# Optimization experiments

Hardware: AMD Instinct MI355X
Metric: run time of the kernel (lower is better)

## Reference

```python
import jax, jax.numpy as jnp
import numpy as np

B, T = 128, 512          # batch, sequence length (padded game length)
F_IN = 19 * 19           # flattened Go board features
H = 128                  # n_hid
P = 19 * 19 + 1          # policy classes: board points + pass


def setup_inputs() -> dict:
    key = jax.random.key(0)
    ks = jax.random.split(key, 8)
    s = 0.05  # init scale
    return {
        "states": jax.random.normal(ks[0], (B, T, F_IN), jnp.float32),
        "moves": jax.random.randint(ks[1], (B, T), 0, P, jnp.int32),
        "values": jax.random.uniform(ks[2], (B, T), jnp.float32, -1.0, 1.0),
        # LSTM layer 0: concat([x, h]) @ W0 + b0, gates [i, f, g, o]
        "W0": jax.random.normal(ks[3], (F_IN + H, 4 * H), jnp.float32) * s,
        "b0": jnp.zeros((4 * H,), jnp.float32),
        # LSTM layer 1
        "W1": jax.random.normal(ks[4], (H + H, 4 * H), jnp.float32) * s,
        "b1": jnp.zeros((4 * H,), jnp.float32),
        # policy head (size**2 + 1 logits), value head (tanh scalar)
        "Wp": jax.random.normal(ks[5], (H, P), jnp.float32) * s,
        "bp": jnp.zeros((P,), jnp.float32),
        "Wv": jax.random.normal(ks[6], (H, 1), jnp.float32) * s,
        "bv": jnp.zeros((1,), jnp.float32),
    }


def _lstm_cell(h, c, x, W, b):
    # TF LSTMCell: z = [x; h] @ W + b, forget bias 1.0
    z = jnp.concatenate([x, h], axis=-1) @ W + b
    i, f, g, o = jnp.split(z, 4, axis=-1)
    c_new = jax.nn.sigmoid(f + 1.0) * c + jax.nn.sigmoid(i) * jnp.tanh(g)
    h_new = jax.nn.sigmoid(o) * jnp.tanh(c_new)
    return h_new, c_new


def reference(states, moves, values, W0, b0, W1, b1, Wp, bp, Wv, bv):
    b = states.shape[0]
    zeros = jnp.zeros((b, H), states.dtype)

    def step(carry, x_t):
        h0, c0, h1, c1 = carry
        h0, c0 = _lstm_cell(h0, c0, x_t, W0, b0)
        h1, c1 = _lstm_cell(h1, c1, h0, W1, b1)
        return (h0, c0, h1, c1), h1

    _, hs = jax.lax.scan(step, (zeros, zeros, zeros, zeros),
                         jnp.swapaxes(states, 0, 1))  # hs: [T, B, H]
    outputs = jnp.swapaxes(hs, 0, 1)                  # [B, T, H]

    policy_logits = outputs @ Wp + bp                 # [B, T, P]
    winners = jnp.tanh(outputs @ Wv + bv)[..., 0]     # [B, T]

    mask = (values != -9.0).astype(jnp.float32)
    n_mask = mask.sum()

    logp = jax.nn.log_softmax(policy_logits, axis=-1)
    xent = -jnp.take_along_axis(logp, moves[..., None].astype(jnp.int32), axis=-1)[..., 0]
    policy_loss = (mask * xent).sum() / n_mask
    value_loss = (mask * jnp.square(winners - values)).sum() / n_mask
    acc = (moves == jnp.argmax(policy_logits, axis=-1).astype(moves.dtype)).astype(jnp.float32).mean()
    return jnp.stack([policy_loss, value_loss, acc])
```

## Files before the change

### kernel.cpp

```cpp
#include <hip/hip_runtime.h>
#include <hip/hip_bf16.h>
#include <stdint.h>


typedef short v8s __attribute__((ext_vector_type(8)));
typedef float v4f __attribute__((ext_vector_type(4)));
typedef int   v8i __attribute__((ext_vector_type(8)));

#define MFMA_B16(a,b,c) __builtin_amdgcn_mfma_f32_16x16x32_bf16((a),(b),(c),0,0,0)
#define MFMA_MX(a,b,c) \
  __builtin_amdgcn_mfma_scale_f32_16x16x128_f8f6f4((a),(b),(c),0,0,0,0x7F7F7F7F,0,0x7F7F7F7F)

#define NT     512
#define FIN    361
#define KP0    384
#define NPC    362
#define NPP    368

#define OFF_Z    ((size_t)0)
#define OFF_H1   ((size_t)83886080)
#define OFF_W0XT ((size_t)100663296)
#define OFF_WPT  ((size_t)101187584)
#define OFF_B0P  ((size_t)101281792)
#define OFF_BPP  ((size_t)101285888)
#define OFF_ACC  ((size_t)101287936)

static __device__ __forceinline__ short f2b(float f) {
  __hip_bfloat16 h = __float2bfloat16(f);
  union { __hip_bfloat16 h; short s; } cv; cv.h = h; return cv.s;
}
static __device__ __forceinline__ float b2f(unsigned int lo16) {
  union { unsigned u; float f; } cv; cv.u = lo16 << 16; return cv.f;
}
static __device__ __forceinline__ unsigned f2e4m3(float f) {
  union { float f; unsigned u; } cv; cv.f = f;
  unsigned s = (cv.u >> 31) << 7;
  float a = fabsf(f);
  a = fminf(a, 448.f);
  unsigned code;
  if (a >= 0.015625f) {
    union { float f; unsigned u; } m; m.f = a;
    unsigned u = m.u + 0x7FFFF + ((m.u >> 20) & 1);
    code = (u >> 20) - 960;
    if (code > 126u) code = 126u;
  } else {
    code = (unsigned)rintf(a * 512.f);
  }
  return s | code;
}
static __device__ __forceinline__ unsigned f2e4m3_fast(float f) {
#if __has_builtin(__builtin_amdgcn_cvt_pk_fp8_f32)
  return (unsigned)__builtin_amdgcn_cvt_pk_fp8_f32(f, f, 0, false) & 0xffu;
#else
  return f2e4m3(f);
#endif
}

static __device__ __forceinline__ void sync_lds() {
  __builtin_amdgcn_sched_barrier(0);
  asm volatile("s_waitcnt lgkmcnt(0)" ::: "memory");
  __builtin_amdgcn_s_barrier();
  __builtin_amdgcn_sched_barrier(0);
}

__global__ __launch_bounds__(256) void k_conv_weights(
    const float* __restrict__ W0, const float* __restrict__ b0,
    const float* __restrict__ Wp, const float* __restrict__ bp,
    char* __restrict__ ws) {
  int idx = blockIdx.x * 256 + threadIdx.x;
  __hip_bfloat16* W0xT = (__hip_bfloat16*)(ws + OFF_W0XT);
  __hip_bfloat16* WpT  = (__hip_bfloat16*)(ws + OFF_WPT);
  float* b0p = (float*)(ws + OFF_B0P);
  float* bpp = (float*)(ws + OFF_BPP);
  float* acc = (float*)(ws + OFF_ACC);

  if (idx < 196608) {
    int np = idx / 384, k = idx - np * 384;
    int n = (np >> 2) + 128 * (np & 3);
    float v = (k < FIN) ? W0[(size_t)k * 512 + n] : 0.f;
    W0xT[idx] = __float2bfloat16(v);
    return;
  }
  idx -= 196608;
  if (idx < 47104) {
    int p = idx >> 7, k = idx & 127;
    WpT[idx] = __float2bfloat16(p < NPC ? Wp[(size_t)k * NPC + p] : 0.f);
    return;
  }
  idx -= 47104;
  if (idx < 512) {
    int n = (idx >> 2) + 128 * (idx & 3);
    b0p[idx] = b0[n] + (((idx & 3) == 1) ? 1.0f : 0.0f);
    return;
  }
  idx -= 512;
  if (idx < NPP) { bpp[idx] = (idx < NPC) ? bp[idx] : -1e30f; return; }
  idx -= NPP;
  if (idx < 4) { acc[idx] = 0.f; return; }
}

template<int KTOT, bool AF32>
__global__ __launch_bounds__(256) void k_gemm(
    const void* __restrict__ Ap, const __hip_bfloat16* __restrict__ BT,
    const float* __restrict__ bias, __hip_bfloat16* __restrict__ C) {
  __shared__ char sm[65536];
  const int tid = threadIdx.x;
  const int l = tid & 63, wm = tid >> 6;
  const int c = l & 15, lg = l >> 4;
  const int m0 = blockIdx.x * 128;
  const int n0 = blockIdx.y * 128;
  constexpr int NS = KTOT / 64;

  uint4 ra[4], rb[4];
  float fa[32];

  auto LD = [&](int ks) {
#pragma unroll
    for (int i = 0; i < 4; i++) {
      int idx = i * 4096 + tid * 16;
      int row = idx >> 7, colb = idx & 127;
      if constexpr (AF32) {
        int r = m0 + row;
        const float* src = (const float*)Ap + ((size_t)(r & 127) * NT + (r >> 7)) * FIN;
        int kb = ks * 64 + (colb >> 1);
#pragma unroll
        for (int u = 0; u < 8; u++) {
          int kf = kb + u;
          fa[i * 8 + u] = (kf < FIN) ? src[kf] : 0.f;
        }
      } else {
        ra[i] = *(const uint4*)((const char*)Ap + ((size_t)(m0 + row) * KTOT + ks * 64) * 2 + colb);
      }
      rb[i] = *(const uint4*)((const char*)BT + ((size_t)(n0 + row) * KTOT + ks * 64) * 2 + colb);
    }
  };
  auto ST = [&](int bsel) {
#pragma unroll
    for (int i = 0; i < 4; i++) {
      int idx = i * 4096 + tid * 16;
      int row = idx >> 7, colb = idx & 127;
      int sw = colb ^ ((row & 7) << 4);
      if constexpr (AF32) {
        v8s w;
#pragma unroll
        for (int u = 0; u < 8; u++) w[u] = f2b(fa[i * 8 + u]);
        *(v8s*)(sm + bsel * 16384 + row * 128 + sw) = w;
      } else {
        *(uint4*)(sm + bsel * 16384 + row * 128 + sw) = ra[i];
      }
      *(uint4*)(sm + 32768 + bsel * 16384 + row * 128 + sw) = rb[i];
    }
  };

  v4f acc[2][8];
  v4f z4 = {0.f, 0.f, 0.f, 0.f};
#pragma unroll
  for (int mt = 0; mt < 2; mt++)
#pragma unroll
    for (int nt = 0; nt < 8; nt++) acc[mt][nt] = z4;

  LD(0); ST(0);
  __syncthreads();
  for (int ks = 0; ks < NS; ks++) {
    if (ks + 1 < NS) LD(ks + 1);
    const int bsel = ks & 1;
#pragma unroll
    for (int kk = 0; kk < 2; kk++) {
      int bir = kk * 64 + lg * 16;
      v8s af[2];
#pragma unroll
      for (int mt = 0; mt < 2; mt++) {
        int row = wm * 32 + mt * 16 + c;
        af[mt] = *(v8s*)(sm + bsel * 16384 + row * 128 + (bir ^ ((row & 7) << 4)));
      }
#pragma unroll
      for (int nt = 0; nt < 8; nt++) {
        int n = nt * 16 + c;
        v8s bf = *(v8s*)(sm + 32768 + bsel * 16384 + n * 128 + (bir ^ ((n & 7) << 4)));
#pragma unroll
        for (int mt = 0; mt < 2; mt++) acc[mt][nt] = MFMA_B16(af[mt], bf, acc[mt][nt]);
      }
    }
    if (ks + 1 < NS) ST((ks + 1) & 1);
    __syncthreads();
  }

#pragma unroll
  for (int mt = 0; mt < 2; mt++)
#pragma unroll
    for (int nt = 0; nt < 8; nt++) {
      int colp = n0 + nt * 16 + c;
      float bs = bias[colp];
#pragma unroll
      for (int j = 0; j < 4; j++) {
        int row = m0 + wm * 32 + mt * 16 + lg * 4 + j;
        C[(size_t)row * 512 + colp] = __float2bfloat16(acc[mt][nt][j] + bs);
      }
    }
}

__global__ __launch_bounds__(1024, 4) void k_scan12(
    const __hip_bfloat16* __restrict__ Z, const float* __restrict__ W0f,
    const float* __restrict__ W1f, const float* __restrict__ b1,
    __hip_bfloat16* __restrict__ h1out) {
  __shared__ char sm[8192];
  const int tid = threadIdx.x;
  const int l = tid & 63, wv = tid >> 6;
  const int c = l & 15, lg = l >> 4;
  const int role = wv >> 3, rw = wv & 7;
  const int B0 = blockIdx.x * 4;
  const int m_ = 16 * rw + c;
  const int row = 4 * lg;
  v4f z4 = {0.f, 0.f, 0.f, 0.f};
  const int wf8 = row * 128 + (((m_ >> 3) ^ row) << 3) + (m_ & 7);

  for (int e = tid * 4; e < 8192; e += 1024 * 4) *(int*)(sm + e) = 0;

  auto AFRAG = [&](int base) -> v8i {
    union { unsigned long long q[4]; v8i v; } u;
#pragma unroll
    for (int t = 0; t < 4; t++)
      u.q[t] = *(const unsigned long long*)(
          sm + base + c * 128 + ((((lg * 4 + t) ^ c) & 15) << 3));
    return u.v;
  };

  if (role == 0) {
    v8i breg[4];
#pragma unroll
    for (int g = 0; g < 4; g++) {
      int n = g * 128 + m_;
      union { unsigned long long q[4]; v8i v; } u;
#pragma unroll
      for (int t = 0; t < 4; t++) {
        unsigned long long w = 0ull;
#pragma unroll
        for (int j = 0; j < 8; j++) {
          int k = lg * 32 + t * 8 + j;
          w |= (unsigned long long)f2e4m3(W0f[(size_t)(FIN + k) * 512 + n]) << (8 * j);
        }
        u.q[t] = w;
      }
      breg[g] = u.v;
    }

    uint2 zA, zB, zC;
    auto ZLD = [&](int t) -> uint2 {
      return *(const uint2*)(Z + ((size_t)t * 128 + B0 + lg) * 512 + m_ * 4);
    };
    zA = ZLD(0); zB = ZLD(1);
    float cst = 0.f;
    __syncthreads();

    for (int s = 0; s < NT; s++) {
      v8i av = AFRAG(((s + 1) & 1) * 2048);
      v4f acc[4];
#pragma unroll
      for (int g = 0; g < 4; g++) acc[g] = z4;
#pragma unroll
      for (int g = 0; g < 4; g++) acc[g] = MFMA_MX(av, breg[g], acc[g]);
      if (s + 2 < NT) zC = ZLD(s + 2);

      float xi = acc[0][0] + b2f(zA.x & 0xffffu);
      float xf = acc[1][0] + b2f(zA.x >> 16);
      float xg = acc[2][0] + b2f(zA.y & 0xffffu);
      float xo = acc[3][0] + b2f(zA.y >> 16);
      float ei = __expf(-xi);
      float ef = __expf(-xf);
      float eg = __expf(2.f * xg);
      float eo = __expf(-xo);
      float cn = cst * __builtin_amdgcn_rcpf(1.f + ef)
               + (eg - 1.f) * __builtin_amdgcn_rcpf((1.f + ei) * (eg + 1.f));
      cst = cn;
      float ec = __expf(2.f * cn);
      float hv = (ec - 1.f) * __builtin_amdgcn_rcpf((1.f + eo) * (ec + 1.f));
      *(unsigned char*)(sm + (s & 1) * 2048 + wf8) = (unsigned char)f2e4m3_fast(hv);
      zA = zB; zB = zC;
      sync_lds();
    }
    sync_lds();
  } else {
    v8i bregH[4], bregX[4];
#pragma unroll
    for (int g = 0; g < 4; g++) {
      int n = g * 128 + m_;
      union { unsigned long long q[4]; v8i v; } uh, ux;
#pragma unroll
      for (int t = 0; t < 4; t++) {
        unsigned long long wh = 0ull, wx = 0ull;
#pragma unroll
        for (int j = 0; j < 8; j++) {
          int k = lg * 32 + t * 8 + j;
          wh |= (unsigned long long)f2e4m3(W1f[(size_t)(128 + k) * 512 + n]) << (8 * j);
          wx |= (unsigned long long)f2e4m3(W1f[(size_t)k * 512 + n]) << (8 * j);
        }
        uh.q[t] = wh; ux.q[t] = wx;
      }
      bregH[g] = uh.v; bregX[g] = ux.v;
    }
    float bq[4];
#pragma unroll
    for (int g = 0; g < 4; g++)
      bq[g] = b1[g * 128 + m_] + ((g == 1) ? 1.0f : 0.0f);
    float cst = 0.f;
    __syncthreads();
    sync_lds();

    for (int s = 1; s <= NT; s++) {
      v8i ah = AFRAG(4096 + (s & 1) * 2048);
      v8i ax = AFRAG(((s + 1) & 1) * 2048);
      v4f acc[4];
#pragma unroll
      for (int g = 0; g < 4; g++) acc[g] = (v4f){bq[g], bq[g], bq[g], bq[g]};
#pragma unroll
      for (int g = 0; g < 4; g++) acc[g] = MFMA_MX(ah, bregH[g], acc[g]);
#pragma unroll
      for (int g = 0; g < 4; g++) acc[g] = MFMA_MX(ax, bregX[g], acc[g]);

      float xi = acc[0][0], xf = acc[1][0], xg = acc[2][0], xo = acc[3][0];
      float ei = __expf(-xi);
      float ef = __expf(-xf);
      float eg = __expf(2.f * xg);
      float eo = __expf(-xo);
      float cn = cst * __builtin_amdgcn_rcpf(1.f + ef)
               + (eg - 1.f) * __builtin_amdgcn_rcpf((1.f + ei) * (eg + 1.f));
      cst = cn;
      float ec = __expf(2.f * cn);
      float hv = (ec - 1.f) * __builtin_amdgcn_rcpf((1.f + eo) * (ec + 1.f));
      *(unsigned char*)(sm + 4096 + ((s + 1) & 1) * 2048 + wf8) =
          (unsigned char)f2e4m3_fast(hv);
      union { short s; __hip_bfloat16 h; } cv; cv.s = f2b(hv);
      h1out[((size_t)(s - 1) * 128 + B0 + lg) * 128 + m_] = cv.h;
      sync_lds();
    }
  }
}

__global__ __launch_bounds__(256) void k_heads(
    const __hip_bfloat16* __restrict__ Hh, const __hip_bfloat16* __restrict__ WpT,
    const float* __restrict__ bpp, const float* __restrict__ Wv,
    const float* __restrict__ bv, const int* __restrict__ moves,
    const float* __restrict__ values, float* __restrict__ accum) {
  __shared__ char sm[110592];
  const int tid = threadIdx.x;
  const int l = tid & 63, wm = tid >> 6;
  const int c = l & 15, lg = l >> 4;
  const int r0 = blockIdx.x * 64;

#pragma unroll
  for (int i = 0; i < 4; i++) {
    int idx = i * 4096 + tid * 16;
    int row = idx >> 8, colb = idx & 255;
    uint4 v = *(const uint4*)((const char*)Hh + (size_t)r0 * 256 + idx);
    *(uint4*)(sm + row * 256 + (colb ^ ((row & 7) << 4))) = v;
  }
#pragma unroll
  for (int i = 0; i < 23; i++) {
    int idx = i * 4096 + tid * 16;
    int row = idx >> 8, colb = idx & 255;
    uint4 v = *(const uint4*)((const char*)WpT + idx);
    *(uint4*)(sm + 16384 + row * 256 + (colb ^ ((row & 7) << 4))) = v;
  }
  __syncthreads();

  v4f acc[23];
  v4f z4 = {0.f, 0.f, 0.f, 0.f};
#pragma unroll
  for (int q = 0; q < 23; q++) acc[q] = z4;
#pragma unroll
  for (int kk = 0; kk < 4; kk++) {
    int bir = kk * 64 + lg * 16;
    int ar = wm * 16 + c;
    v8s a = *(v8s*)(sm + ar * 256 + (bir ^ ((ar & 7) << 4)));
#pragma unroll
    for (int q = 0; q < 23; q++) {
      int n = q * 16 + c;
      v8s b = *(v8s*)(sm + 16384 + n * 256 + (bir ^ ((n & 7) << 4)));
      acc[q] = MFMA_B16(a, b, acc[q]);
    }
  }
  float bq[23];
#pragma unroll
  for (int q = 0; q < 23; q++) bq[q] = bpp[q * 16 + c];

  float tp = 0.f, tv = 0.f, ta = 0.f, tn = 0.f;
#pragma unroll
  for (int j = 0; j < 4; j++) {
    int rloc = lg * 4 + j;
    int r = r0 + wm * 16 + rloc;
    int t = r >> 7, b = r & 127;
    int mv = moves[(size_t)b * NT + t];
    float val = values[(size_t)b * NT + t];
    float msk = (val != -9.0f) ? 1.f : 0.f;

    float pmax = -3.0e38f;
#pragma unroll
    for (int q = 0; q < 23; q++) pmax = fmaxf(pmax, acc[q][j] + bq[q]);
#pragma unroll
    for (int d = 1; d < 16; d <<= 1) pmax = fmaxf(pmax, __shfl_xor(pmax, d, 64));
    float ps = 0.f;
#pragma unroll
    for (int q = 0; q < 23; q++) ps += __expf((acc[q][j] + bq[q]) - pmax);
#pragma unroll
    for (int d = 1; d < 16; d <<= 1) ps += __shfl_xor(ps, d, 64);
    float lse = pmax + __logf(ps);

    int qm = mv >> 4, cm = mv & 15;
    float mlv = 0.f;
#pragma unroll
    for (int q = 0; q < 23; q++) if (q == qm) mlv = acc[q][j] + bq[q];
    mlv = __shfl(mlv, (l & 48) + cm, 64);
    float xent = lse - mlv;

    float amx = -3.0e38f; int aix = 0;
#pragma unroll
    for (int q = 0; q < 23; q++) {
      float v = acc[q][j] + bq[q];
      if (v > amx) { amx = v; aix = q * 16 + c; }
    }
#pragma unroll
    for (int d = 1; d < 16; d <<= 1) {
      float ov = __shfl_xor(amx, d, 64);
      int oi = __shfl_xor(aix, d, 64);
      if (ov > amx || (ov == amx && oi < aix)) { amx = ov; aix = oi; }
    }

    float pd = 0.f;
    int vrow = wm * 16 + rloc;
#pragma unroll
    for (int i = 0; i < 8; i++) {
      int k = c * 8 + i;
      short hv = *(short*)(sm + vrow * 256 + ((k * 2) ^ ((vrow & 7) << 4)));
      pd += b2f((unsigned short)hv) * Wv[k];
    }
#pragma unroll
    for (int d = 1; d < 16; d <<= 1) pd += __shfl_xor(pd, d, 64);
    float eo = __expf(2.f * (pd + bv[0]));
    float win = (eo - 1.f) * __builtin_amdgcn_rcpf(eo + 1.f);
    float dv = win - val;

    if (c == 0) {
      tp += msk * xent;
      tv += msk * dv * dv;
      ta += (aix == mv) ? 1.f : 0.f;
      tn += msk;
    }
  }
  tp += __shfl_xor(tp, 16, 64); tp += __shfl_xor(tp, 32, 64);
  tv += __shfl_xor(tv, 16, 64); tv += __shfl_xor(tv, 32, 64);
  ta += __shfl_xor(ta, 16, 64); ta += __shfl_xor(ta, 32, 64);
  tn += __shfl_xor(tn, 16, 64); tn += __shfl_xor(tn, 32, 64);
  if (l == 0) {
    atomicAdd(accum + 0, tp);
    atomicAdd(accum + 1, tv);
    atomicAdd(accum + 2, ta);
    atomicAdd(accum + 3, tn);
  }
}

__global__ void k_final(const float* __restrict__ accum, float* __restrict__ out) {
  if (threadIdx.x == 0) {
    float nm = accum[3];
    out[0] = accum[0] / nm;
    out[1] = accum[1] / nm;
    out[2] = accum[2] / 65536.0f;
  }
}

extern "C" void kernel_launch(void* const* d_in, const int* in_sizes, int n_in,
                              void* d_out, int out_size, void* d_ws, size_t ws_size,
                              hipStream_t stream) {
  (void)in_sizes; (void)n_in; (void)out_size; (void)ws_size;
  const float* states = (const float*)d_in[0];
  const int*   moves  = (const int*)d_in[1];
  const float* values = (const float*)d_in[2];
  const float* W0 = (const float*)d_in[3];
  const float* b0 = (const float*)d_in[4];
  const float* W1 = (const float*)d_in[5];
  const float* b1 = (const float*)d_in[6];
  const float* Wp = (const float*)d_in[7];
  const float* bp = (const float*)d_in[8];
  const float* Wv = (const float*)d_in[9];
  const float* bv = (const float*)d_in[10];
  char* ws = (char*)d_ws;

  __hip_bfloat16* zbuf = (__hip_bfloat16*)(ws + OFF_Z);
  __hip_bfloat16* h1   = (__hip_bfloat16*)(ws + OFF_H1);
  __hip_bfloat16* W0xT = (__hip_bfloat16*)(ws + OFF_W0XT);
  __hip_bfloat16* WpT  = (__hip_bfloat16*)(ws + OFF_WPT);
  float* b0p = (float*)(ws + OFF_B0P);
  float* bpp = (float*)(ws + OFF_BPP);
  float* acc = (float*)(ws + OFF_ACC);

  k_conv_weights<<<956, 256, 0, stream>>>(W0, b0, Wp, bp, ws);
  k_gemm<KP0, true><<<dim3(512, 4), 256, 0, stream>>>(states, W0xT, b0p, zbuf);
  k_scan12<<<32, 1024, 0, stream>>>(zbuf, W0, W1, b1, h1);
  k_heads<<<1024, 256, 0, stream>>>(h1, WpT, bpp, Wv, bv, moves, values, acc);
  k_final<<<1, 1, 0, stream>>>(acc, (float*)d_out);
}
```

Baseline: 829.5 us.

## Fuse input GEMM, recurrent scan and heads into one persistent kernel with flags

```diff
diff --git a/kernel.cpp b/kernel.cpp
--- a/kernel.cpp
+++ b/kernel.cpp
@@ -16,14 +16,18 @@
 #define KP0    384
 #define NPC    362
 #define NPP    368
-
-#define OFF_Z    ((size_t)0)
-#define OFF_H1   ((size_t)83886080)
-#define OFF_W0XT ((size_t)100663296)
-#define OFF_WPT  ((size_t)101187584)
-#define OFF_B0P  ((size_t)101281792)
-#define OFF_BPP  ((size_t)101285888)
-#define OFF_ACC  ((size_t)101287936)
+#define AG __HIP_MEMORY_SCOPE_AGENT
+
+#define OFF_Z     ((size_t)0)
+#define OFF_H1    ((size_t)83886080)
+#define OFF_W0XT  ((size_t)100663296)
+#define OFF_WPT   ((size_t)101187584)
+#define OFF_B0P   ((size_t)101281792)
+#define OFF_BPP   ((size_t)101285888)
+#define OFF_ACC   ((size_t)101287936)
+#define OFF_ZDONE ((size_t)101288000)
+#define OFF_DONE  ((size_t)101290048)
+#define OFF_TK    ((size_t)101292096)
 
 static __device__ __forceinline__ short f2b(float f) {
   __hip_bfloat16 h = __float2bfloat16(f);
@@ -31,6 +35,9 @@
 }
 static __device__ __forceinline__ float b2f(unsigned int lo16) {
   union { unsigned u; float f; } cv; cv.u = lo16 << 16; return cv.f;
+}
+static __device__ __forceinline__ float u2f(unsigned int bits) {
+  union { unsigned u; float f; } cv; cv.u = bits; return cv.f;
 }
 static __device__ __forceinline__ unsigned f2e4m3(float f) {
   union { float f; unsigned u; } cv; cv.f = f;
@@ -62,6 +69,12 @@
   __builtin_amdgcn_s_barrier();
   __builtin_amdgcn_sched_barrier(0);
 }
+static __device__ __forceinline__ void sync_vm() {
+  __builtin_amdgcn_sched_barrier(0);
+  asm volatile("s_waitcnt vmcnt(0) lgkmcnt(0)" ::: "memory");
+  __builtin_amdgcn_s_barrier();
+  __builtin_amdgcn_sched_barrier(0);
+}
 
 __global__ __launch_bounds__(256) void k_conv_weights(
     const float* __restrict__ W0, const float* __restrict__ b0,
@@ -73,6 +86,9 @@
   float* b0p = (float*)(ws + OFF_B0P);
   float* bpp = (float*)(ws + OFF_BPP);
   float* acc = (float*)(ws + OFF_ACC);
+  int* zdone = (int*)(ws + OFF_ZDONE);
+  int* done  = (int*)(ws + OFF_DONE);
+  int* tk    = (int*)(ws + OFF_TK);
 
   if (idx < 196608) {
     int np = idx / 384, k = idx - np * 384;
@@ -97,364 +113,408 @@
   if (idx < NPP) { bpp[idx] = (idx < NPC) ? bp[idx] : -1e30f; return; }
   idx -= NPP;
   if (idx < 4) { acc[idx] = 0.f; return; }
-}
-
-template<int KTOT, bool AF32>
-__global__ __launch_bounds__(256) void k_gemm(
-    const void* __restrict__ Ap, const __hip_bfloat16* __restrict__ BT,
-    const float* __restrict__ bias, __hip_bfloat16* __restrict__ C) {
-  __shared__ char sm[65536];
-  const int tid = threadIdx.x;
-  const int l = tid & 63, wm = tid >> 6;
-  const int c = l & 15, lg = l >> 4;
-  const int m0 = blockIdx.x * 128;
-  const int n0 = blockIdx.y * 128;
-  constexpr int NS = KTOT / 64;
-
-  uint4 ra[4], rb[4];
-  float fa[32];
-
-  auto LD = [&](int ks) {
-#pragma unroll
-    for (int i = 0; i < 4; i++) {
-      int idx = i * 4096 + tid * 16;
-      int row = idx >> 7, colb = idx & 127;
-      if constexpr (AF32) {
-        int r = m0 + row;
-        const float* src = (const float*)Ap + ((size_t)(r & 127) * NT + (r >> 7)) * FIN;
-        int kb = ks * 64 + (colb >> 1);
-#pragma unroll
-        for (int u = 0; u < 8; u++) {
-          int kf = kb + u;
-          fa[i * 8 + u] = (kf < FIN) ? src[kf] : 0.f;
-        }
-      } else {
-        ra[i] = *(const uint4*)((const char*)Ap + ((size_t)(m0 + row) * KTOT + ks * 64) * 2 + colb);
-      }
-      rb[i] = *(const uint4*)((const char*)BT + ((size_t)(n0 + row) * KTOT + ks * 64) * 2 + colb);
-    }
-  };
-  auto ST = [&](int bsel) {
-#pragma unroll
-    for (int i = 0; i < 4; i++) {
-      int idx = i * 4096 + tid * 16;
-      int row = idx >> 7, colb = idx & 127;
-      int sw = colb ^ ((row & 7) << 4);
-      if constexpr (AF32) {
-        v8s w;
-#pragma unroll
-        for (int u = 0; u < 8; u++) w[u] = f2b(fa[i * 8 + u]);
-        *(v8s*)(sm + bsel * 16384 + row * 128 + sw) = w;
-      } else {
-        *(uint4*)(sm + bsel * 16384 + row * 128 + sw) = ra[i];
-      }
-      *(uint4*)(sm + 32768 + bsel * 16384 + row * 128 + sw) = rb[i];
-    }
-  };
-
-  v4f acc[2][8];
-  v4f z4 = {0.f, 0.f, 0.f, 0.f};
-#pragma unroll
-  for (int mt = 0; mt < 2; mt++)
-#pragma unroll
-    for (int nt = 0; nt < 8; nt++) acc[mt][nt] = z4;
-
-  LD(0); ST(0);
-  __syncthreads();
-  for (int ks = 0; ks < NS; ks++) {
-    if (ks + 1 < NS) LD(ks + 1);
-    const int bsel = ks & 1;
-#pragma unroll
-    for (int kk = 0; kk < 2; kk++) {
-      int bir = kk * 64 + lg * 16;
-      v8s af[2];
-#pragma unroll
-      for (int mt = 0; mt < 2; mt++) {
-        int row = wm * 32 + mt * 16 + c;
-        af[mt] = *(v8s*)(sm + bsel * 16384 + row * 128 + (bir ^ ((row & 7) << 4)));
-      }
-#pragma unroll
-      for (int nt = 0; nt < 8; nt++) {
-        int n = nt * 16 + c;
-        v8s bf = *(v8s*)(sm + 32768 + bsel * 16384 + n * 128 + (bir ^ ((n & 7) << 4)));
-#pragma unroll
-        for (int mt = 0; mt < 2; mt++) acc[mt][nt] = MFMA_B16(af[mt], bf, acc[mt][nt]);
-      }
-    }
-    if (ks + 1 < NS) ST((ks + 1) & 1);
-    __syncthreads();
-  }
-
-#pragma unroll
-  for (int mt = 0; mt < 2; mt++)
-#pragma unroll
-    for (int nt = 0; nt < 8; nt++) {
-      int colp = n0 + nt * 16 + c;
-      float bs = bias[colp];
-#pragma unroll
-      for (int j = 0; j < 4; j++) {
-        int row = m0 + wm * 32 + mt * 16 + lg * 4 + j;
-        C[(size_t)row * 512 + colp] = __float2bfloat16(acc[mt][nt][j] + bs);
-      }
-    }
-}
-
-__global__ __launch_bounds__(1024, 4) void k_scan12(
-    const __hip_bfloat16* __restrict__ Z, const float* __restrict__ W0f,
+  idx -= 4;
+  if (idx < 512) { zdone[idx] = 0; return; }
+  idx -= 512;
+  if (idx < 512) { done[idx] = 0; return; }
+  idx -= 512;
+  if (idx < 8) { tk[idx] = 0; return; }
+}
+
+__global__ __launch_bounds__(1024, 1) void k_mega(
+    const float* __restrict__ states, const int* __restrict__ moves,
+    const float* __restrict__ values, const float* __restrict__ W0f,
     const float* __restrict__ W1f, const float* __restrict__ b1,
-    __hip_bfloat16* __restrict__ h1out) {
-  __shared__ char sm[8192];
+    const float* __restrict__ Wv, const float* __restrict__ bv,
+    char* __restrict__ ws) {
+  __shared__ char sm[110656];
   const int tid = threadIdx.x;
   const int l = tid & 63, wv = tid >> 6;
   const int c = l & 15, lg = l >> 4;
-  const int role = wv >> 3, rw = wv & 7;
-  const int B0 = blockIdx.x * 4;
-  const int m_ = 16 * rw + c;
-  const int row = 4 * lg;
-  v4f z4 = {0.f, 0.f, 0.f, 0.f};
-  const int wf8 = row * 128 + (((m_ >> 3) ^ row) << 3) + (m_ & 7);
-
-  for (int e = tid * 4; e < 8192; e += 1024 * 4) *(int*)(sm + e) = 0;
-
-  auto AFRAG = [&](int base) -> v8i {
-    union { unsigned long long q[4]; v8i v; } u;
-#pragma unroll
-    for (int t = 0; t < 4; t++)
-      u.q[t] = *(const unsigned long long*)(
-          sm + base + c * 128 + ((((lg * 4 + t) ^ c) & 15) << 3));
-    return u.v;
-  };
-
-  if (role == 0) {
-    v8i breg[4];
-#pragma unroll
-    for (int g = 0; g < 4; g++) {
-      int n = g * 128 + m_;
+
+  __hip_bfloat16* Zb  = (__hip_bfloat16*)(ws + OFF_Z);
+  unsigned short* h1u = (unsigned short*)(ws + OFF_H1);
+  const __hip_bfloat16* W0xT = (const __hip_bfloat16*)(ws + OFF_W0XT);
+  const __hip_bfloat16* WpT  = (const __hip_bfloat16*)(ws + OFF_WPT);
+  const float* b0p = (const float*)(ws + OFF_B0P);
+  const float* bpp = (const float*)(ws + OFF_BPP);
+  float* accum = (float*)(ws + OFF_ACC);
+  int* zdone = (int*)(ws + OFF_ZDONE);
+  int* done  = (int*)(ws + OFF_DONE);
+  int* tk    = (int*)(ws + OFF_TK);
+
+  if (blockIdx.x < 32) {
+    const int role = wv >> 3, rw = wv & 7;
+    const int B0 = blockIdx.x * 4;
+    const int m_ = 16 * rw + c;
+    const int row = 4 * lg;
+    const int wf8 = row * 128 + (((m_ >> 3) ^ row) << 3) + (m_ & 7);
+
+    for (int e = tid * 4; e < 8192; e += 1024 * 4) *(int*)(sm + e) = 0;
+
+    auto AFRAG = [&](int base) -> v8i {
       union { unsigned long long q[4]; v8i v; } u;
 #pragma unroll
-      for (int t = 0; t < 4; t++) {
-        unsigned long long w = 0ull;
-#pragma unroll
-        for (int j = 0; j < 8; j++) {
-          int k = lg * 32 + t * 8 + j;
-          w |= (unsigned long long)f2e4m3(W0f[(size_t)(FIN + k) * 512 + n]) << (8 * j);
-        }
-        u.q[t] = w;
-      }
-      breg[g] = u.v;
-    }
-
-    uint2 zA, zB, zC;
-    auto ZLD = [&](int t) -> uint2 {
-      return *(const uint2*)(Z + ((size_t)t * 128 + B0 + lg) * 512 + m_ * 4);
+      for (int t = 0; t < 4; t++)
+        u.q[t] = *(const unsigned long long*)(
+            sm + base + c * 128 + ((((lg * 4 + t) ^ c) & 15) << 3));
+      return u.v;
     };
-    zA = ZLD(0); zB = ZLD(1);
-    float cst = 0.f;
-    __syncthreads();
-
-    for (int s = 0; s < NT; s++) {
-      v8i av = AFRAG(((s + 1) & 1) * 2048);
+
+    if (role == 0) {
+      v8i breg[4];
+#pragma unroll
+      for (int g = 0; g < 4; g++) {
+        int n = g * 128 + m_;
+        union { unsigned long long q[4]; v8i v; } u;
+#pragma unroll
+        for (int t = 0; t < 4; t++) {
+          unsigned long long w = 0ull;
+#pragma unroll
+          for (int j = 0; j < 8; j++) {
+            int k = lg * 32 + t * 8 + j;
+            w |= (unsigned long long)f2e4m3(W0f[(size_t)(FIN + k) * 512 + n]) << (8 * j);
+          }
+          u.q[t] = w;
+        }
+        breg[g] = u.v;
+      }
+      for (int q = 0; q < 4; q++)
+        while (__hip_atomic_load(&zdone[q], __ATOMIC_ACQUIRE, AG) < 4)
+          __builtin_amdgcn_s_sleep(8);
+
+      auto ZLD = [&](int t) -> uint2 {
+        unsigned long long v = __hip_atomic_load(
+            (const unsigned long long*)Zb +
+            (((size_t)t * 128 + B0 + lg) * 512 + m_ * 4) / 4,
+            __ATOMIC_RELAXED, AG);
+        union { unsigned long long q; uint2 u; } cv; cv.q = v; return cv.u;
+      };
+      uint2 zA = ZLD(0), zB = ZLD(1), zC;
+      float cst = 0.f;
       v4f acc[4];
 #pragma unroll
-      for (int g = 0; g < 4; g++) acc[g] = z4;
-#pragma unroll
-      for (int g = 0; g < 4; g++) acc[g] = MFMA_MX(av, breg[g], acc[g]);
-      if (s + 2 < NT) zC = ZLD(s + 2);
-
-      float xi = acc[0][0] + b2f(zA.x & 0xffffu);
-      float xf = acc[1][0] + b2f(zA.x >> 16);
-      float xg = acc[2][0] + b2f(zA.y & 0xffffu);
-      float xo = acc[3][0] + b2f(zA.y >> 16);
-      float ei = __expf(-xi);
-      float ef = __expf(-xf);
-      float eg = __expf(2.f * xg);
-      float eo = __expf(-xo);
-      float cn = cst * __builtin_amdgcn_rcpf(1.f + ef)
-               + (eg - 1.f) * __builtin_amdgcn_rcpf((1.f + ei) * (eg + 1.f));
-      cst = cn;
-      float ec = __expf(2.f * cn);
-      float hv = (ec - 1.f) * __builtin_amdgcn_rcpf((1.f + eo) * (ec + 1.f));
-      *(unsigned char*)(sm + (s & 1) * 2048 + wf8) = (unsigned char)f2e4m3_fast(hv);
-      zA = zB; zB = zC;
+      for (int g = 0; g < 4; g++) acc[g] = (v4f){0.f, 0.f, 0.f, 0.f};
+      int zseen = 4;
+      const bool p0 = (tid == 0);
+      __syncthreads();
+
+      for (int s = 0; s < NT; s++) {
+        int fl = 0;
+        if (p0 && zseen < NT)
+          fl = __hip_atomic_load(&zdone[zseen], __ATOMIC_RELAXED, AG);
+        v8i av = AFRAG(((s + 1) & 1) * 2048);
+        acc[0][0] = u2f(zA.x << 16);
+        acc[1][0] = u2f(zA.x & 0xffff0000u);
+        acc[2][0] = u2f(zA.y << 16);
+        acc[3][0] = u2f(zA.y & 0xffff0000u);
+#pragma unroll
+        for (int g = 0; g < 4; g++) acc[g] = MFMA_MX(av, breg[g], acc[g]);
+        if (s + 2 < NT) zC = ZLD(s + 2);
+
+        float xi = acc[0][0], xf = acc[1][0], xg = acc[2][0], xo = acc[3][0];
+        float ei = __expf(-xi);
+        float ef = __expf(-xf);
+        float eg = __expf(2.f * xg);
+        float eo = __expf(-xo);
+        float cn = cst * __builtin_amdgcn_rcpf(1.f + ef)
+                 + (eg - 1.f) * __builtin_amdgcn_rcpf((1.f + ei) * (eg + 1.f));
+        cst = cn;
+        float ec = __expf(2.f * cn);
+        float hv = (ec - 1.f) * __builtin_amdgcn_rcpf((1.f + eo) * (ec + 1.f));
+        *(unsigned char*)(sm + (s & 1) * 2048 + wf8) = (unsigned char)f2e4m3_fast(hv);
+        zA = zB; zB = zC;
+        if (p0) {
+          if (zseen < NT && fl >= 4) zseen++;
+          int need = s + 4; if (need > NT) need = NT;
+          while (zseen < need) {
+            if (__hip_atomic_load(&zdone[zseen], __ATOMIC_ACQUIRE, AG) >= 4) zseen++;
+            else __builtin_amdgcn_s_sleep(8);
+          }
+        }
+        sync_lds();
+      }
       sync_lds();
-    }
-    sync_lds();
-  } else {
-    v8i bregH[4], bregX[4];
-#pragma unroll
-    for (int g = 0; g < 4; g++) {
-      int n = g * 128 + m_;
-      union { unsigned long long q[4]; v8i v; } uh, ux;
-#pragma unroll
-      for (int t = 0; t < 4; t++) {
-        unsigned long long wh = 0ull, wx = 0ull;
-#pragma unroll
-        for (int j = 0; j < 8; j++) {
-          int k = lg * 32 + t * 8 + j;
-          wh |= (unsigned long long)f2e4m3(W1f[(size_t)(128 + k) * 512 + n]) << (8 * j);
-          wx |= (unsigned long long)f2e4m3(W1f[(size_t)k * 512 + n]) << (8 * j);
-        }
-        uh.q[t] = wh; ux.q[t] = wx;
-      }
-      bregH[g] = uh.v; bregX[g] = ux.v;
-    }
-    float bq[4];
-#pragma unroll
-    for (int g = 0; g < 4; g++)
-      bq[g] = b1[g * 128 + m_] + ((g == 1) ? 1.0f : 0.0f);
-    float cst = 0.f;
-    __syncthreads();
-    sync_lds();
-
-    for (int s = 1; s <= NT; s++) {
-      v8i ah = AFRAG(4096 + (s & 1) * 2048);
-      v8i ax = AFRAG(((s + 1) & 1) * 2048);
+    } else {
+      v8i bregH[4], bregX[4];
+#pragma unroll
+      for (int g = 0; g < 4; g++) {
+        int n = g * 128 + m_;
+        union { unsigned long long q[4]; v8i v; } uh, ux;
+#pragma unroll
+        for (int t = 0; t < 4; t++) {
+          unsigned long long wh = 0ull, wx = 0ull;
+#pragma unroll
+          for (int j = 0; j < 8; j++) {
+            int k = lg * 32 + t * 8 + j;
+            wh |= (unsigned long long)f2e4m3(W1f[(size_t)(128 + k) * 512 + n]) << (8 * j);
+            wx |= (unsigned long long)f2e4m3(W1f[(size_t)k * 512 + n]) << (8 * j);
+          }
+          uh.q[t] = wh; ux.q[t] = wx;
+        }
+        bregH[g] = uh.v; bregX[g] = ux.v;
+      }
+      float bq[4];
+#pragma unroll
+      for (int g = 0; g < 4; g++)
+        bq[g] = b1[g * 128 + m_] + ((g == 1) ? 1.0f : 0.0f);
+      float cst = 0.f;
       v4f acc[4];
 #pragma unroll
       for (int g = 0; g < 4; g++) acc[g] = (v4f){bq[g], bq[g], bq[g], bq[g]};
-#pragma unroll
-      for (int g = 0; g < 4; g++) acc[g] = MFMA_MX(ah, bregH[g], acc[g]);
-#pragma unroll
-      for (int g = 0; g < 4; g++) acc[g] = MFMA_MX(ax, bregX[g], acc[g]);
-
-      float xi = acc[0][0], xf = acc[1][0], xg = acc[2][0], xo = acc[3][0];
-      float ei = __expf(-xi);
-      float ef = __expf(-xf);
-      float eg = __expf(2.f * xg);
-      float eo = __expf(-xo);
-      float cn = cst * __builtin_amdgcn_rcpf(1.f + ef)
-               + (eg - 1.f) * __builtin_amdgcn_rcpf((1.f + ei) * (eg + 1.f));
-      cst = cn;
-      float ec = __expf(2.f * cn);
-      float hv = (ec - 1.f) * __builtin_amdgcn_rcpf((1.f + eo) * (ec + 1.f));
-      *(unsigned char*)(sm + 4096 + ((s + 1) & 1) * 2048 + wf8) =
-          (unsigned char)f2e4m3_fast(hv);
-      union { short s; __hip_bfloat16 h; } cv; cv.s = f2b(hv);
-      h1out[((size_t)(s - 1) * 128 + B0 + lg) * 128 + m_] = cv.h;
+      const bool pd = (tid == 512);
+      __syncthreads();
       sync_lds();
-    }
-  }
-}
-
-__global__ __launch_bounds__(256) void k_heads(
-    const __hip_bfloat16* __restrict__ Hh, const __hip_bfloat16* __restrict__ WpT,
-    const float* __restrict__ bpp, const float* __restrict__ Wv,
-    const float* __restrict__ bv, const int* __restrict__ moves,
-    const float* __restrict__ values, float* __restrict__ accum) {
-  __shared__ char sm[110592];
-  const int tid = threadIdx.x;
-  const int l = tid & 63, wm = tid >> 6;
-  const int c = l & 15, lg = l >> 4;
-  const int r0 = blockIdx.x * 64;
-
-#pragma unroll
-  for (int i = 0; i < 4; i++) {
-    int idx = i * 4096 + tid * 16;
-    int row = idx >> 8, colb = idx & 255;
-    uint4 v = *(const uint4*)((const char*)Hh + (size_t)r0 * 256 + idx);
-    *(uint4*)(sm + row * 256 + (colb ^ ((row & 7) << 4))) = v;
-  }
-#pragma unroll
-  for (int i = 0; i < 23; i++) {
-    int idx = i * 4096 + tid * 16;
-    int row = idx >> 8, colb = idx & 255;
-    uint4 v = *(const uint4*)((const char*)WpT + idx);
-    *(uint4*)(sm + 16384 + row * 256 + (colb ^ ((row & 7) << 4))) = v;
-  }
-  __syncthreads();
-
-  v4f acc[23];
-  v4f z4 = {0.f, 0.f, 0.f, 0.f};
-#pragma unroll
-  for (int q = 0; q < 23; q++) acc[q] = z4;
-#pragma unroll
-  for (int kk = 0; kk < 4; kk++) {
-    int bir = kk * 64 + lg * 16;
-    int ar = wm * 16 + c;
-    v8s a = *(v8s*)(sm + ar * 256 + (bir ^ ((ar & 7) << 4)));
-#pragma unroll
-    for (int q = 0; q < 23; q++) {
-      int n = q * 16 + c;
-      v8s b = *(v8s*)(sm + 16384 + n * 256 + (bir ^ ((n & 7) << 4)));
-      acc[q] = MFMA_B16(a, b, acc[q]);
-    }
-  }
-  float bq[23];
-#pragma unroll
-  for (int q = 0; q < 23; q++) bq[q] = bpp[q * 16 + c];
-
-  float tp = 0.f, tv = 0.f, ta = 0.f, tn = 0.f;
-#pragma unroll
-  for (int j = 0; j < 4; j++) {
-    int rloc = lg * 4 + j;
-    int r = r0 + wm * 16 + rloc;
-    int t = r >> 7, b = r & 127;
-    int mv = moves[(size_t)b * NT + t];
-    float val = values[(size_t)b * NT + t];
-    float msk = (val != -9.0f) ? 1.f : 0.f;
-
-    float pmax = -3.0e38f;
-#pragma unroll
-    for (int q = 0; q < 23; q++) pmax = fmaxf(pmax, acc[q][j] + bq[q]);
-#pragma unroll
-    for (int d = 1; d < 16; d <<= 1) pmax = fmaxf(pmax, __shfl_xor(pmax, d, 64));
-    float ps = 0.f;
-#pragma unroll
-    for (int q = 0; q < 23; q++) ps += __expf((acc[q][j] + bq[q]) - pmax);
-#pragma unroll
-    for (int d = 1; d < 16; d <<= 1) ps += __shfl_xor(ps, d, 64);
-    float lse = pmax + __logf(ps);
-
-    int qm = mv >> 4, cm = mv & 15;
-    float mlv = 0.f;
-#pragma unroll
-    for (int q = 0; q < 23; q++) if (q == qm) mlv = acc[q][j] + bq[q];
-    mlv = __shfl(mlv, (l & 48) + cm, 64);
-    float xent = lse - mlv;
-
-    float amx = -3.0e38f; int aix = 0;
-#pragma unroll
-    for (int q = 0; q < 23; q++) {
-      float v = acc[q][j] + bq[q];
-      if (v > amx) { amx = v; aix = q * 16 + c; }
-    }
-#pragma unroll
-    for (int d = 1; d < 16; d <<= 1) {
-      float ov = __shfl_xor(amx, d, 64);
-      int oi = __shfl_xor(aix, d, 64);
-      if (ov > amx || (ov == amx && oi < aix)) { amx = ov; aix = oi; }
-    }
-
-    float pd = 0.f;
-    int vrow = wm * 16 + rloc;
-#pragma unroll
-    for (int i = 0; i < 8; i++) {
-      int k = c * 8 + i;
-      short hv = *(short*)(sm + vrow * 256 + ((k * 2) ^ ((vrow & 7) << 4)));
-      pd += b2f((unsigned short)hv) * Wv[k];
-    }
-#pragma unroll
-    for (int d = 1; d < 16; d <<= 1) pd += __shfl_xor(pd, d, 64);
-    float eo = __expf(2.f * (pd + bv[0]));
-    float win = (eo - 1.f) * __builtin_amdgcn_rcpf(eo + 1.f);
-    float dv = win - val;
-
-    if (c == 0) {
-      tp += msk * xent;
-      tv += msk * dv * dv;
-      ta += (aix == mv) ? 1.f : 0.f;
-      tn += msk;
-    }
-  }
-  tp += __shfl_xor(tp, 16, 64); tp += __shfl_xor(tp, 32, 64);
-  tv += __shfl_xor(tv, 16, 64); tv += __shfl_xor(tv, 32, 64);
-  ta += __shfl_xor(ta, 16, 64); ta += __shfl_xor(ta, 32, 64);
-  tn += __shfl_xor(tn, 16, 64); tn += __shfl_xor(tn, 32, 64);
-  if (l == 0) {
-    atomicAdd(accum + 0, tp);
-    atomicAdd(accum + 1, tv);
-    atomicAdd(accum + 2, ta);
-    atomicAdd(accum + 3, tn);
+
+      for (int s = 1; s <= NT; s++) {
+        v8i ah = AFRAG(4096 + (s & 1) * 2048);
+        v8i ax = AFRAG(((s + 1) & 1) * 2048);
+#pragma unroll
+        for (int g = 0; g < 4; g++) acc[g][0] = bq[g];
+#pragma unroll
+        for (int g = 0; g < 4; g++) acc[g] = MFMA_MX(ah, bregH[g], acc[g]);
+#pragma unroll
+        for (int g = 0; g < 4; g++) acc[g] = MFMA_MX(ax, bregX[g], acc[g]);
+
+        float xi = acc[0][0], xf = acc[1][0], xg = acc[2][0], xo = acc[3][0];
+        float ei = __expf(-xi);
+        float ef = __expf(-xf);
+        float eg = __expf(2.f * xg);
+        float eo = __expf(-xo);
+        float cn = cst * __builtin_amdgcn_rcpf(1.f + ef)
+                 + (eg - 1.f) * __builtin_amdgcn_rcpf((1.f + ei) * (eg + 1.f));
+        cst = cn;
+        float ec = __expf(2.f * cn);
+        float hv = (ec - 1.f) * __builtin_amdgcn_rcpf((1.f + eo) * (ec + 1.f));
+        *(unsigned char*)(sm + 4096 + ((s + 1) & 1) * 2048 + wf8) =
+            (unsigned char)f2e4m3_fast(hv);
+        __hip_atomic_store(
+            h1u + ((size_t)(s - 1) * 128 + B0 + lg) * 128 + m_,
+            (unsigned short)f2b(hv), __ATOMIC_RELAXED, AG);
+        sync_vm();
+        if (pd) __hip_atomic_fetch_add(&done[s - 1], 1, __ATOMIC_RELEASE, AG);
+      }
+    }
+    return;
+  }
+
+  int* tks = (int*)(sm + 110592);
+  const int wm = wv;
+
+  for (;;) {
+    if (tid == 0) *tks = atomicAdd(&tk[0], 1);
+    __syncthreads();
+    int i = *tks;
+    __syncthreads();
+    if (i >= 2048) break;
+    const int bx = i >> 2, by = i & 3;
+    const int m0 = bx * 128, n0 = by * 128;
+    v4f ga[2][8];
+    if (tid < 256) {
+#pragma unroll
+      for (int mt = 0; mt < 2; mt++)
+#pragma unroll
+        for (int nt = 0; nt < 8; nt++) ga[mt][nt] = (v4f){0.f, 0.f, 0.f, 0.f};
+    }
+    for (int ks = 0; ks < 6; ks++) {
+      __syncthreads();
+      if (tid < 256) {
+#pragma unroll
+        for (int ii = 0; ii < 4; ii++) {
+          int idx = ii * 4096 + tid * 16;
+          int rr = idx >> 7, colb = idx & 127;
+          int r = m0 + rr;
+          const float* src = states + ((size_t)(r & 127) * NT + (r >> 7)) * FIN;
+          int kb = ks * 64 + (colb >> 1);
+          v8s w;
+#pragma unroll
+          for (int u = 0; u < 8; u++) {
+            int kf = kb + u;
+            w[u] = f2b((kf < FIN) ? src[kf] : 0.f);
+          }
+          *(v8s*)(sm + rr * 128 + (colb ^ ((rr & 7) << 4))) = w;
+          uint4 rbv = *(const uint4*)((const char*)W0xT +
+              ((size_t)(n0 + rr) * KP0 + ks * 64) * 2 + colb);
+          *(uint4*)(sm + 16384 + rr * 128 + (colb ^ ((rr & 7) << 4))) = rbv;
+        }
+      }
+      __syncthreads();
+      if (tid < 256) {
+#pragma unroll
+        for (int kk = 0; kk < 2; kk++) {
+          int bir = kk * 64 + lg * 16;
+          v8s af[2];
+#pragma unroll
+          for (int mt = 0; mt < 2; mt++) {
+            int rr = wm * 32 + mt * 16 + c;
+            af[mt] = *(v8s*)(sm + rr * 128 + (bir ^ ((rr & 7) << 4)));
+          }
+#pragma unroll
+          for (int nt = 0; nt < 8; nt++) {
+            int n = nt * 16 + c;
+            v8s bf = *(v8s*)(sm + 16384 + n * 128 + (bir ^ ((n & 7) << 4)));
+#pragma unroll
+            for (int mt = 0; mt < 2; mt++) ga[mt][nt] = MFMA_B16(af[mt], bf, ga[mt][nt]);
+          }
+        }
+      }
+    }
+    if (tid < 256) {
+#pragma unroll
+      for (int mt = 0; mt < 2; mt++)
+#pragma unroll
+        for (int nt = 0; nt < 8; nt++) {
+          int colp = n0 + nt * 16 + c;
+          float bs = b0p[colp];
+#pragma unroll
+          for (int j = 0; j < 4; j++) {
+            int rp = m0 + wm * 32 + mt * 16 + lg * 4 + j;
+            __hip_atomic_store((unsigned short*)Zb + (size_t)rp * 512 + colp,
+                               (unsigned short)f2b(ga[mt][nt][j] + bs),
+                               __ATOMIC_RELAXED, AG);
+          }
+        }
+    }
+    __syncthreads();
+    if (tid == 0) __hip_atomic_fetch_add(&zdone[bx], 1, __ATOMIC_RELEASE, AG);
+  }
+
+  if (tid < 256) {
+#pragma unroll
+    for (int ii = 0; ii < 23; ii++) {
+      int idx = ii * 4096 + tid * 16;
+      int rr = idx >> 8, colb = idx & 255;
+      uint4 v = *(const uint4*)((const char*)WpT + idx);
+      *(uint4*)(sm + 16384 + rr * 256 + (colb ^ ((rr & 7) << 4))) = v;
+    }
+  }
+  for (;;) {
+    if (tid == 0) *tks = atomicAdd(&tk[1], 1);
+    __syncthreads();
+    int j = *tks;
+    __syncthreads();
+    if (j >= 1024) break;
+    const int r0 = j * 64;
+    const int tt = r0 >> 7;
+    if (tid == 0) {
+      while (__hip_atomic_load(&done[tt], __ATOMIC_ACQUIRE, AG) < 32)
+        __builtin_amdgcn_s_sleep(8);
+    }
+    __syncthreads();
+    if (tid < 256) {
+#pragma unroll
+      for (int ii = 0; ii < 8; ii++) {
+        int idx = ii * 2048 + tid * 8;
+        int rr = idx >> 8, colb = idx & 255;
+        unsigned long long v = __hip_atomic_load(
+            (const unsigned long long*)h1u + (size_t)r0 * 32 + (idx >> 3),
+            __ATOMIC_RELAXED, AG);
+        *(unsigned long long*)(sm + rr * 256 + (colb ^ ((rr & 7) << 4))) = v;
+      }
+    }
+    __syncthreads();
+    if (tid < 256) {
+      float m_[4], l_[4], mlv[4], amx[4]; int aix[4];
+      int mv_[4]; float val_[4];
+#pragma unroll
+      for (int jj = 0; jj < 4; jj++) {
+        int r = r0 + wm * 16 + lg * 4 + jj;
+        int t = r >> 7, b = r & 127;
+        mv_[jj] = moves[(size_t)b * NT + t];
+        val_[jj] = values[(size_t)b * NT + t];
+        m_[jj] = -3.0e38f; l_[jj] = 0.f; mlv[jj] = 0.f;
+        amx[jj] = -3.0e38f; aix[jj] = 0;
+      }
+#pragma unroll
+      for (int ch = 0; ch < 2; ch++) {
+        const int q0 = ch * 12;
+        const int nq = ch ? 11 : 12;
+        v4f acc[12];
+#pragma unroll
+        for (int q = 0; q < 12; q++) acc[q] = (v4f){0.f, 0.f, 0.f, 0.f};
+#pragma unroll
+        for (int kk = 0; kk < 4; kk++) {
+          int bir = kk * 64 + lg * 16;
+          int ar = wm * 16 + c;
+          v8s a = *(v8s*)(sm + ar * 256 + (bir ^ ((ar & 7) << 4)));
+          for (int q = 0; q < nq; q++) {
+            int n = (q0 + q) * 16 + c;
+            v8s bfr = *(v8s*)(sm + 16384 + n * 256 + (bir ^ ((n & 7) << 4)));
+            acc[q] = MFMA_B16(a, bfr, acc[q]);
+          }
+        }
+        float bqc[12];
+        for (int q = 0; q < nq; q++) bqc[q] = bpp[(q0 + q) * 16 + c];
+#pragma unroll
+        for (int jj = 0; jj < 4; jj++) {
+          float pm = -3.0e38f;
+          for (int q = 0; q < nq; q++) pm = fmaxf(pm, acc[q][jj] + bqc[q]);
+#pragma unroll
+          for (int d = 1; d < 16; d <<= 1) pm = fmaxf(pm, __shfl_xor(pm, d, 64));
+          float nm = fmaxf(m_[jj], pm);
+          float sc = __expf(m_[jj] - nm);
+          float ps = 0.f;
+          for (int q = 0; q < nq; q++) ps += __expf((acc[q][jj] + bqc[q]) - nm);
+#pragma unroll
+          for (int d = 1; d < 16; d <<= 1) ps += __shfl_xor(ps, d, 64);
+          l_[jj] = l_[jj] * sc + ps;
+          m_[jj] = nm;
+          int qm = mv_[jj] >> 4, cm = mv_[jj] & 15;
+          float vvm = 0.f;
+          for (int q = 0; q < nq; q++) if (q0 + q == qm) vvm = acc[q][jj] + bqc[q];
+          vvm = __shfl(vvm, (l & 48) + cm, 64);
+          if (qm >= q0 && qm < q0 + nq) mlv[jj] = vvm;
+          for (int q = 0; q < nq; q++) {
+            float v = acc[q][jj] + bqc[q];
+            if (v > amx[jj]) { amx[jj] = v; aix[jj] = (q0 + q) * 16 + c; }
+          }
+        }
+      }
+      float tp = 0.f, tv = 0.f, ta = 0.f, tn = 0.f;
+#pragma unroll
+      for (int jj = 0; jj < 4; jj++) {
+        float am = amx[jj]; int ai = aix[jj];
+#pragma unroll
+        for (int d = 1; d < 16; d <<= 1) {
+          float ov = __shfl_xor(am, d, 64);
+          int oi = __shfl_xor(ai, d, 64);
+          if (ov > am || (ov == am && oi < ai)) { am = ov; ai = oi; }
+        }
+        float lse = m_[jj] + __logf(l_[jj]);
+        float xent = lse - mlv[jj];
+        float pdv = 0.f;
+        int vrow = wm * 16 + lg * 4 + jj;
+#pragma unroll
+        for (int ii = 0; ii < 8; ii++) {
+          int k = c * 8 + ii;
+          short hvb = *(short*)(sm + vrow * 256 + ((k * 2) ^ ((vrow & 7) << 4)));
+          pdv += b2f((unsigned short)hvb) * Wv[k];
+        }
+#pragma unroll
+        for (int d = 1; d < 16; d <<= 1) pdv += __shfl_xor(pdv, d, 64);
+        float eo = __expf(2.f * (pdv + bv[0]));
+        float win = (eo - 1.f) * __builtin_amdgcn_rcpf(eo + 1.f);
+        float dv = win - val_[jj];
+        float msk = (val_[jj] != -9.0f) ? 1.f : 0.f;
+        if (c == 0) {
+          tp += msk * xent;
+          tv += msk * dv * dv;
+          ta += (ai == mv_[jj]) ? 1.f : 0.f;
+          tn += msk;
+        }
+      }
+      tp += __shfl_xor(tp, 16, 64); tp += __shfl_xor(tp, 32, 64);
+      tv += __shfl_xor(tv, 16, 64); tv += __shfl_xor(tv, 32, 64);
+      ta += __shfl_xor(ta, 16, 64); ta += __shfl_xor(ta, 32, 64);
+      tn += __shfl_xor(tn, 16, 64); tn += __shfl_xor(tn, 32, 64);
+      if (l == 0) {
+        atomicAdd(accum + 0, tp);
+        atomicAdd(accum + 1, tv);
+        atomicAdd(accum + 2, ta);
+        atomicAdd(accum + 3, tn);
+      }
+    }
+    __syncthreads();
   }
 }
 
@@ -484,17 +544,7 @@
   const float* bv = (const float*)d_in[10];
   char* ws = (char*)d_ws;
 
-  __hip_bfloat16* zbuf = (__hip_bfloat16*)(ws + OFF_Z);
-  __hip_bfloat16* h1   = (__hip_bfloat16*)(ws + OFF_H1);
-  __hip_bfloat16* W0xT = (__hip_bfloat16*)(ws + OFF_W0XT);
-  __hip_bfloat16* WpT  = (__hip_bfloat16*)(ws + OFF_WPT);
-  float* b0p = (float*)(ws + OFF_B0P);
-  float* bpp = (float*)(ws + OFF_BPP);
-  float* acc = (float*)(ws + OFF_ACC);
-
-  k_conv_weights<<<956, 256, 0, stream>>>(W0, b0, Wp, bp, ws);
-  k_gemm<KP0, true><<<dim3(512, 4), 256, 0, stream>>>(states, W0xT, b0p, zbuf);
-  k_scan12<<<32, 1024, 0, stream>>>(zbuf, W0, W1, b1, h1);
-  k_heads<<<1024, 256, 0, stream>>>(h1, WpT, bpp, Wv, bv, moves, values, acc);
-  k_final<<<1, 1, 0, stream>>>(acc, (float*)d_out);
-}
+  k_conv_weights<<<960, 256, 0, stream>>>(W0, b0, Wp, bp, ws);
+  k_mega<<<256, 1024, 0, stream>>>(states, moves, values, W0, W1, b1, Wv, bv, ws);
+  k_final<<<1, 1, 0, stream>>>((const float*)(ws + OFF_ACC), (float*)d_out);
+}
```

After: 2.836 ms. +241.8%, slower.

## Replace per-step workgroup barriers with LDS counter flags in LSTM scan

Applied to the files above, without the earlier changes.

```diff
diff --git a/kernel.cpp b/kernel.cpp
--- a/kernel.cpp
+++ b/kernel.cpp
@@ -16,6 +16,7 @@
 #define KP0    384
 #define NPC    362
 #define NPP    368
+#define WGS __HIP_MEMORY_SCOPE_WORKGROUP
 
 #define OFF_Z    ((size_t)0)
 #define OFF_H1   ((size_t)83886080)
@@ -56,11 +57,15 @@
 #endif
 }
 
-static __device__ __forceinline__ void sync_lds() {
-  __builtin_amdgcn_sched_barrier(0);
-  asm volatile("s_waitcnt lgkmcnt(0)" ::: "memory");
-  __builtin_amdgcn_s_barrier();
-  __builtin_amdgcn_sched_barrier(0);
+static __device__ __forceinline__ int wait_ge(int* f, int tgt, int cached) {
+  if (cached >= tgt) return cached;
+  int v = 0;
+  for (int g = 0; g < (1 << 22); ++g) {
+    v = __hip_atomic_load(f, __ATOMIC_ACQUIRE, WGS);
+    if (v >= tgt) return v;
+    __builtin_amdgcn_s_sleep(1);
+  }
+  return v;
 }
 
 __global__ __launch_bounds__(256) void k_conv_weights(
@@ -203,7 +208,7 @@
     const __hip_bfloat16* __restrict__ Z, const float* __restrict__ W0f,
     const float* __restrict__ W1f, const float* __restrict__ b1,
     __hip_bfloat16* __restrict__ h1out) {
-  __shared__ char sm[8192];
+  __shared__ char sm[16512];
   const int tid = threadIdx.x;
   const int l = tid & 63, wv = tid >> 6;
   const int c = l & 15, lg = l >> 4;
@@ -211,10 +216,11 @@
   const int B0 = blockIdx.x * 4;
   const int m_ = 16 * rw + c;
   const int row = 4 * lg;
-  v4f z4 = {0.f, 0.f, 0.f, 0.f};
   const int wf8 = row * 128 + (((m_ >> 3) ^ row) << 3) + (m_ & 7);
-
-  for (int e = tid * 4; e < 8192; e += 1024 * 4) *(int*)(sm + e) = 0;
+  int* c0 = (int*)(sm + 16384);
+  int* c1 = (int*)(sm + 16448);
+
+  for (int e = tid * 4; e < 16512; e += 4096) *(int*)(sm + e) = 0;
 
   auto AFRAG = [&](int base) -> v8i {
     union { unsigned long long q[4]; v8i v; } u;
@@ -250,13 +256,16 @@
     };
     zA = ZLD(0); zB = ZLD(1);
     float cst = 0.f;
+    int c0s = 0, c1s = 0;
     __syncthreads();
 
     for (int s = 0; s < NT; s++) {
-      v8i av = AFRAG(((s + 1) & 1) * 2048);
+      c0s = wait_ge(c0, 8 * s, c0s);
+      if (s >= 4) c1s = wait_ge(c1, 8 * (s - 3), c1s);
+      v8i av = AFRAG(((s + 3) & 3) * 2048);
       v4f acc[4];
 #pragma unroll
-      for (int g = 0; g < 4; g++) acc[g] = z4;
+      for (int g = 0; g < 4; g++) acc[g] = (v4f){0.f, 0.f, 0.f, 0.f};
 #pragma unroll
       for (int g = 0; g < 4; g++) acc[g] = MFMA_MX(av, breg[g], acc[g]);
       if (s + 2 < NT) zC = ZLD(s + 2);
@@ -274,11 +283,11 @@
       cst = cn;
       float ec = __expf(2.f * cn);
       float hv = (ec - 1.f) * __builtin_amdgcn_rcpf((1.f + eo) * (ec + 1.f));
-      *(unsigned char*)(sm + (s & 1) * 2048 + wf8) = (unsigned char)f2e4m3_fast(hv);
+      *(unsigned char*)(sm + (s & 3) * 2048 + wf8) = (unsigned char)f2e4m3_fast(hv);
       zA = zB; zB = zC;
-      sync_lds();
-    }
-    sync_lds();
+      asm volatile("s_waitcnt lgkmcnt(0)" ::: "memory");
+      if (l == 0) __hip_atomic_fetch_add(c0, 1, __ATOMIC_RELEASE, WGS);
+    }
   } else {
     v8i bregH[4], bregX[4];
 #pragma unroll
@@ -303,12 +312,14 @@
     for (int g = 0; g < 4; g++)
       bq[g] = b1[g * 128 + m_] + ((g == 1) ? 1.0f : 0.0f);
     float cst = 0.f;
+    int c0s = 0, c1s = 0;
     __syncthreads();
-    sync_lds();
-
-    for (int s = 1; s <= NT; s++) {
-      v8i ah = AFRAG(4096 + (s & 1) * 2048);
-      v8i ax = AFRAG(((s + 1) & 1) * 2048);
+
+    for (int t = 1; t <= NT; t++) {
+      c0s = wait_ge(c0, 8 * t, c0s);
+      c1s = wait_ge(c1, 8 * (t - 1), c1s);
+      v8i ah = AFRAG(8192 + ((t + 2) & 3) * 2048);
+      v8i ax = AFRAG(((t + 3) & 3) * 2048);
       v4f acc[4];
 #pragma unroll
       for (int g = 0; g < 4; g++) acc[g] = (v4f){bq[g], bq[g], bq[g], bq[g]};
@@ -327,11 +338,12 @@
       cst = cn;
       float ec = __expf(2.f * cn);
       float hv = (ec - 1.f) * __builtin_amdgcn_rcpf((1.f + eo) * (ec + 1.f));
-      *(unsigned char*)(sm + 4096 + ((s + 1) & 1) * 2048 + wf8) =
+      *(unsigned char*)(sm + 8192 + ((t - 1) & 3) * 2048 + wf8) =
           (unsigned char)f2e4m3_fast(hv);
       union { short s; __hip_bfloat16 h; } cv; cv.s = f2b(hv);
-      h1out[((size_t)(s - 1) * 128 + B0 + lg) * 128 + m_] = cv.h;
-      sync_lds();
+      h1out[((size_t)(t - 1) * 128 + B0 + lg) * 128 + m_] = cv.h;
+      asm volatile("s_waitcnt lgkmcnt(0)" ::: "memory");
+      if (l == 0) __hip_atomic_fetch_add(c1, 1, __ATOMIC_RELEASE, WGS);
     }
   }
 }
```

Result: slower. 899.5 us (+8.4%).
